# Kernel tuning notes

Measured on AMD Instinct MI355X. Metric: run time of the kernel, lower is better.

The kernel has to match this reference:

```python
import jax, jax.numpy as jnp
import numpy as np

N_SAMPLES = 2 ** 15          # 32768
STEP = 256                   # transform_step_size
WIN = 2048                   # transform/synthesis window
N_FRAMES = N_SAMPLES // STEP # 128
N_COEFFS = WIN // 2 + 1      # 1025
DILATIONS = (1, 2, 4, 8, 16, 32, 64, 1)


def hann(n):
    return 0.5 - 0.5 * jnp.cos(2.0 * jnp.pi * jnp.arange(n, dtype=jnp.float32) / n)


def transform(audio):
    # audio: (B, 1, N) -> magnitude STFT (B, 1024, 128)
    x = audio[:, 0, :]
    x = jnp.pad(x, ((0, 0), (0, WIN - STEP)))  # pad so n_frames == N_SAMPLES // STEP
    idx = np.arange(N_FRAMES)[:, None] * STEP + np.arange(WIN)[None, :]
    frames = x[:, idx] * hann(WIN)
    spec = jnp.abs(jnp.fft.rfft(frames, norm='ortho'))   # (B, F, 1025)
    return spec[..., : N_COEFFS - 1].transpose(0, 2, 1)  # (B, 1024, F)


def conv1x1(x, w, b):
    # x: (B, I, T), w: (O, I, 1), b: (O,)
    return jnp.einsum('oi,bit->bot', w[:, :, 0], x) + b[None, :, None]


def anticausal_block(x, w, b, dilation):
    # kernel_size=2 anti-causal dilated conv: looks at t and t+dilation (pad future)
    x_fut = jnp.pad(x, ((0, 0), (0, 0), (0, dilation)))[:, :, dilation:]
    y = (jnp.einsum('oi,bit->bot', w[:, :, 0], x)
         + jnp.einsum('oi,bit->bot', w[:, :, 1], x_fut)
         + b[None, :, None])
    y = jax.nn.leaky_relu(y, 0.2)
    y = y + x
    # do_norm: per-example max-norm
    y = y / (jnp.max(jnp.abs(y), axis=(1, 2), keepdims=True) + 1e-8)
    return y


def upsample_with_holes(x, desired_size):
    # zero-stuffing upsample: out[..., ::step] = x
    b, c, t = x.shape
    step = desired_size // t
    out = jnp.zeros((b, c, desired_size), x.dtype)
    return out.at[:, :, ::step].set(x)


def freq_domain_resonance(coeffs):
    # coeffs: (1, C, 1025) in [0, 1); per-frame decay = repeated spectral multiply
    c = jnp.clip(coeffs, 0.0, 0.9999)
    exps = jnp.arange(1, N_FRAMES + 1, dtype=coeffs.dtype)
    mags = c[:, :, None, :] ** exps[None, None, :, None]     # (1, C, F, 1025)
    frames = jnp.fft.irfft(mags, n=WIN) * hann(WIN)
    hop = WIN // 2
    total = hop * (N_FRAMES - 1) + WIN
    idx = np.arange(N_FRAMES)[:, None] * hop + np.arange(WIN)[None, :]
    out = jnp.zeros(frames.shape[:2] + (total,), frames.dtype)
    out = out.at[:, :, idx].add(frames)                      # overlap-add
    return out[..., :N_SAMPLES]                              # (1, C, N)


def fft_convolve(a, b):
    # circular-free conv via zero-padding to 2N, keep first N (matches repo fft_convolve)
    n = a.shape[-1]
    spec = jnp.fft.rfft(a, n=2 * n) * jnp.fft.rfft(b, n=2 * n)
    return jnp.fft.irfft(spec, n=2 * n)[..., :n]


def reference(audio, proj_in_w, proj_in_b, blocks_w, blocks_b,
              proj_sparse_w, proj_sparse_b, proj_dense_w, proj_dense_b, resonances):
    spec = transform(audio)                         # (B, 1024, 128)
    h = conv1x1(spec, proj_in_w, proj_in_b)         # (B, 32, 128)
    acc = jnp.zeros_like(h)
    for i, d in enumerate(DILATIONS):               # fixed 8-block stack
        h = anticausal_block(h, blocks_w[i], blocks_b[i], d)
        acc = acc + h
    x = conv1x1(acc, proj_sparse_w, proj_sparse_b)  # (B, 256, 128)
    sparse = jax.nn.relu(x)
    x = conv1x1(sparse, proj_dense_w, proj_dense_b) # (B, 32, 128)
    x = upsample_with_holes(x, N_SAMPLES)           # (B, 32, 32768)
    res = freq_domain_resonance(resonances)         # (1, 32, 32768), broadcast over B
    y = fft_convolve(x, res)                        # (B, 32, 32768)
    y = jnp.sum(y, axis=1, keepdims=True)           # (B, 1, 32768)
    return y, sparse


def setup_inputs() -> dict:
    key = jax.random.key(0)
    ks = jax.random.split(key, 12)
    u = lambda k, shape: jax.random.uniform(k, shape, jnp.float32, -0.05, 0.05)
    return {
        'audio': jax.random.normal(ks[0], (32, 1, N_SAMPLES), jnp.float32),
        'proj_in_w': u(ks[1], (32, 1024, 1)),
        'proj_in_b': jnp.zeros((32,), jnp.float32),
        'blocks_w': u(ks[2], (8, 32, 32, 2)),
        'blocks_b': jnp.zeros((8, 32), jnp.float32),
        'proj_sparse_w': u(ks[3], (256, 32, 1)),
        'proj_sparse_b': jnp.zeros((256,), jnp.float32),
        'proj_dense_w': u(ks[4], (32, 256, 1)),
        'proj_dense_b': jnp.zeros((32,), jnp.float32),
        'resonances': jax.random.uniform(ks[5], (1, 32, N_COEFFS), jnp.float32, 0.0, 1.0),
    }
```

## Files before the change

kernel.cpp:

```cpp
#include <hip/hip_runtime.h>

#define PI_F 3.14159265358979323846f

typedef short bf16x8 __attribute__((ext_vector_type(8)));
typedef float f32x4 __attribute__((ext_vector_type(4)));

#define MFMA16(acc, a, b) \
  acc = __builtin_amdgcn_mfma_f32_16x16x32_bf16(a, b, acc, 0, 0, 0)

#define WS_SPEC   0u
#define WS_H0     4194304u
#define WS_ACC    4325376u
#define WS_V      4456448u
#define WS_WTIN   4587520u
#define WS_WST    4620288u
#define WS_WDT    4628480u
#define WS_FRAMES 4636672u
#define WS_RES    6733824u

__device__ __forceinline__ void fft2048_stages(float2* buf, int tid) {
  for (int stage = 0; stage < 11; ++stage) {
    int half = 1 << stage;
    float base = -PI_F / (float)half;
    for (int t = tid; t < 1024; t += 256) {
      int j  = t & (half - 1);
      int i0 = ((t >> stage) << (stage + 1)) + j;
      int i1 = i0 + half;
      float s, c;
      __sincosf(base * (float)j, &s, &c);
      float2 u = buf[i0];
      float2 w = buf[i1];
      float tr = c * w.x - s * w.y;
      float ti = c * w.y + s * w.x;
      buf[i0] = make_float2(u.x + tr, u.y + ti);
      buf[i1] = make_float2(u.x - tr, u.y - ti);
    }
    __syncthreads();
  }
}

__global__ __launch_bounds__(256) void k_fft(const float* __restrict__ audio,
                                             const float* __restrict__ resin,
                                             float* __restrict__ spec,
                                             float* __restrict__ frames) {
  __shared__ float2 buf[2048];
  int blk = blockIdx.x;
  if (blk < 2048) {
    int b  = blk >> 6;
    int f0 = (blk & 63) * 2;
    for (int j = threadIdx.x; j < 2048; j += 256) {
      float h = 0.5f - 0.5f * __cosf(0.0030679615757712823f * (float)j);
      int i1 = f0 * 256 + j;
      int i2 = i1 + 256;
      float a1 = (i1 < 32768) ? audio[b * 32768 + i1] : 0.f;
      float a2 = (i2 < 32768) ? audio[b * 32768 + i2] : 0.f;
      buf[__brev((unsigned)j) >> 21] = make_float2(a1 * h, a2 * h);
    }
    __syncthreads();
    fft2048_stages(buf, threadIdx.x);
    const float scale = 0.5f * 0.022097086912079608f;
    for (int k = threadIdx.x; k < 1024; k += 256) {
      float2 zk = buf[k];
      float2 zn = buf[(2048 - k) & 2047];
      float f1r = zk.x + zn.x, f1i = zk.y - zn.y;
      float f2r = zk.y + zn.y, f2i = zk.x - zn.x;
      spec[(b * 128 + f0) * 1024 + k]     = sqrtf(f1r * f1r + f1i * f1i) * scale;
      spec[(b * 128 + f0 + 1) * 1024 + k] = sqrtf(f2r * f2r + f2i * f2i) * scale;
    }
  } else {
    int r = blk - 2048;
    int c = r >> 4;
    int g = r & 15;
    float e1 = (float)(2 * g + 1);
    for (int k = threadIdx.x; k < 2048; k += 256) {
      int kk = (k <= 1024) ? k : 2048 - k;
      float cv = resin[c * 1025 + kk];
      cv = fminf(fmaxf(cv, 0.f), 0.9999f);
      float m1 = __powf(cv, e1);
      float m2 = m1 * cv;
      buf[__brev((unsigned)k) >> 21] = make_float2(m1, m2);
    }
    __syncthreads();
    fft2048_stages(buf, threadIdx.x);
    for (int j = threadIdx.x; j < 2048; j += 256) {
      float h  = 0.5f - 0.5f * __cosf(0.0030679615757712823f * (float)j);
      float sc = h * (1.f / 2048.f);
      float2 z = buf[j];
      frames[(c * 32 + 2 * g) * 2048 + j]     = z.x * sc;
      frames[(c * 32 + 2 * g + 1) * 2048 + j] = z.y * sc;
    }
  }
}

__global__ __launch_bounds__(256) void k_prep(const float* __restrict__ Win,
                                              const float* __restrict__ Ws,
                                              const float* __restrict__ Wd,
                                              const float* __restrict__ bwIn,
                                              float* __restrict__ WT,
                                              float* __restrict__ WsT,
                                              float* __restrict__ WdT,
                                              short* __restrict__ Whg,
                                              short* __restrict__ Wlg) {
  int i = blockIdx.x * 256 + threadIdx.x;
  if (i < 32768) { int o = i >> 10, k = i & 1023; WT[k * 32 + o] = Win[i]; }
  if (i < 8192)  { int o2 = i >> 5, m = i & 31;   WsT[m * 256 + o2] = Ws[i]; }
  if (i < 8192)  { int c = i >> 8, o2 = i & 255;  WdT[o2 * 32 + c] = Wd[i]; }
  if (i < 16384) {
    int w = i & 1, m = (i >> 1) & 31, o = (i >> 6) & 31, s = i >> 11;
    float val = bwIn[i];
    unsigned bits = __float_as_uint(val);
    float rem = val - __uint_as_float(bits & 0xffff0000u);
    int row = (s * 2 + w) * 32 + o;
    Whg[row * 32 + m] = (short)(bits >> 16);
    Wlg[row * 32 + m] = (short)(__float_as_uint(rem) >> 16);
  }
}

__global__ __launch_bounds__(256) void k_proj_in(const float* __restrict__ spec,
                                                 const float* __restrict__ WT,
                                                 const float* __restrict__ bias,
                                                 float* __restrict__ h0) {
  __shared__ float specL[8][1024];
  __shared__ float red[32][8][8];
  int b  = blockIdx.x >> 4;
  int t0 = (blockIdx.x & 15) * 8;
  for (int i = threadIdx.x; i < 8192; i += 256) {
    int tt = i >> 10, k = i & 1023;
    specL[tt][k] = spec[(b * 128 + t0 + tt) * 1024 + k];
  }
  __syncthreads();
  int o = threadIdx.x & 31, p = threadIdx.x >> 5;
  float part[8] = {0.f,0.f,0.f,0.f,0.f,0.f,0.f,0.f};
  for (int i = 0; i < 128; ++i) {
    int k = p * 128 + ((i + p * 4) & 127);
    float w = WT[k * 32 + o];
#pragma unroll
    for (int tt = 0; tt < 8; ++tt) part[tt] += w * specL[tt][k];
  }
#pragma unroll
  for (int tt = 0; tt < 8; ++tt) red[o][tt][p] = part[tt];
  __syncthreads();
  int oo = threadIdx.x >> 3, tt2 = threadIdx.x & 7;
  float s = bias[oo];
#pragma unroll
  for (int p2 = 0; p2 < 8; ++p2) s += red[oo][tt2][p2];
  h0[b * 4096 + oo * 128 + t0 + tt2] = s;
}

__global__ __launch_bounds__(1024) void k_chain(const float* __restrict__ h0,
                                                const short* __restrict__ Whg,
                                                const short* __restrict__ Wlg,
                                                const float* __restrict__ bb,
                                                float* __restrict__ accout) {
  __shared__ __align__(16) short Hh[192 * 40];
  __shared__ __align__(16) short Hl[192 * 40];
  __shared__ float Hf[128 * 33];
  __shared__ float bL[256];
  __shared__ float red[16];
  int b = blockIdx.x, tid = threadIdx.x;

  for (int i = tid; i < 4096; i += 1024) {
    int t = i & 127;
    int o = i >> 7;
    float val = h0[b * 4096 + i];
    Hf[t * 33 + o] = val;
    unsigned bits = __float_as_uint(val);
    float rem = val - __uint_as_float(bits & 0xffff0000u);
    Hh[t * 40 + o] = (short)(bits >> 16);
    Hl[t * 40 + o] = (short)(__float_as_uint(rem) >> 16);
  }
  for (int i = tid; i < 64 * 40; i += 1024) {
    Hh[128 * 40 + i] = 0;
    Hl[128 * 40 + i] = 0;
  }
  if (tid < 256) bL[tid] = bb[tid];
  __syncthreads();

  int wave = tid >> 6, lane = tid & 63;
  int quad = lane >> 4, l15 = lane & 15;
  int t0 = (wave & 7) * 16, o0 = (wave >> 3) * 16;
  int tD = t0 + quad * 4;
  int oD = o0 + l15;

  const bf16x8* Hh8 = (const bf16x8*)Hh;
  const bf16x8* Hl8 = (const bf16x8*)Hl;
  const bf16x8* Wh8 = (const bf16x8*)Whg;
  const bf16x8* Wl8 = (const bf16x8*)Wlg;

  float accsum[4] = {0.f, 0.f, 0.f, 0.f};
  const int DIL[8] = {1, 2, 4, 8, 16, 32, 64, 1};

#pragma unroll
  for (int s = 0; s < 8; ++s) {
    int arow = t0 + l15;
    int frow = arow + DIL[s];
    bf16x8 Ah = Hh8[arow * 5 + quad];
    bf16x8 Al = Hl8[arow * 5 + quad];
    bf16x8 Fh = Hh8[frow * 5 + quad];
    bf16x8 Fl = Hl8[frow * 5 + quad];
    int w0row = ((s * 2 + 0) * 32 + oD) * 4 + quad;
    int w1row = ((s * 2 + 1) * 32 + oD) * 4 + quad;
    bf16x8 B0h = Wh8[w0row], B0l = Wl8[w0row];
    bf16x8 B1h = Wh8[w1row], B1l = Wl8[w1row];
    float bias = bL[s * 32 + oD];
    f32x4 acc = {bias, bias, bias, bias};
    MFMA16(acc, Ah, B0h); MFMA16(acc, Ah, B0l); MFMA16(acc, Al, B0h);
    MFMA16(acc, Fh, B1h); MFMA16(acc, Fh, B1l); MFMA16(acc, Fl, B1h);
    float hnew[4], lmax = 0.f;
#pragma unroll
    for (int r = 0; r < 4; ++r) {
      float sv = acc[r];
      sv = (sv > 0.f) ? sv : 0.2f * sv;
      sv += Hf[(tD + r) * 33 + oD];
      hnew[r] = sv;
      lmax = fmaxf(lmax, fabsf(sv));
    }
#pragma unroll
    for (int off = 32; off > 0; off >>= 1)
      lmax = fmaxf(lmax, __shfl_down(lmax, off, 64));
    if (lane == 0) red[wave] = lmax;
    __syncthreads();
    float mx = red[0];
#pragma unroll
    for (int i = 1; i < 16; ++i) mx = fmaxf(mx, red[i]);
    float nm = 1.f / (mx + 1e-8f);
#pragma unroll
    for (int r = 0; r < 4; ++r) {
      float hv = hnew[r] * nm;
      accsum[r] += hv;
      int t = tD + r;
      Hf[t * 33 + oD] = hv;
      unsigned bits = __float_as_uint(hv);
      float rem = hv - __uint_as_float(bits & 0xffff0000u);
      Hh[t * 40 + oD] = (short)(bits >> 16);
      Hl[t * 40 + oD] = (short)(__float_as_uint(rem) >> 16);
    }
    __syncthreads();
  }
#pragma unroll
  for (int r = 0; r < 4; ++r)
    accout[b * 4096 + (tD + r) * 32 + oD] = accsum[r];
}

__global__ __launch_bounds__(256) void k_sparse_dense(const float* __restrict__ acc,
                                                      const float* __restrict__ WsT,
                                                      const float* __restrict__ bs,
                                                      const float* __restrict__ WdT,
                                                      const float* __restrict__ bd,
                                                      float* __restrict__ out_sparse,
                                                      float* __restrict__ v) {
  __shared__ float accL[32];
  __shared__ float sL[256];
  __shared__ float red[8][32];
  int b = blockIdx.x >> 7, t = blockIdx.x & 127;
  int tid = threadIdx.x;
  if (tid < 32) accL[tid] = acc[b * 4096 + t * 32 + tid];
  __syncthreads();
  float s = bs[tid];
  for (int m = 0; m < 32; ++m) s += WsT[m * 256 + tid] * accL[m];
  s = fmaxf(s, 0.f);
  out_sparse[b * 32768 + tid * 128 + t] = s;
  sL[tid] = s;
  __syncthreads();
  int c = tid & 31, p = tid >> 5;
  float part = 0.f;
  for (int j = 0; j < 32; ++j) {
    int o2 = p * 32 + j;
    part += WdT[o2 * 32 + c] * sL[o2];
  }
  red[p][c] = part;
  __syncthreads();
  if (tid < 32) {
    float vv = bd[tid];
    for (int p2 = 0; p2 < 8; ++p2) vv += red[p2][tid];
    v[b * 4096 + tid * 128 + t] = vv;
  }
}

__global__ __launch_bounds__(256) void k_res_assemble(const float* __restrict__ frames,
                                                      float* __restrict__ res) {
  int i = blockIdx.x * 256 + threadIdx.x;
  int c = i >> 15, s = i & 32767;
  int g = s >> 10, j0 = s & 1023;
  float v = frames[(c * 32 + g) * 2048 + j0];
  if (g > 0) v += frames[(c * 32 + g - 1) * 2048 + j0 + 1024];
  res[i] = v;
}

__global__ __launch_bounds__(256) void k_bpack(const float* __restrict__ res,
                                               short* __restrict__ Bh,
                                               short* __restrict__ Bl) {
  int c = blockIdx.x >> 4, o = blockIdx.x & 15;
  int r = threadIdx.x;
  bf16x8 hv, lv;
#pragma unroll
  for (int j = 0; j < 8; ++j) {
    float val = res[c * 32768 + (8 * o + j) * 256 + r];
    unsigned bits = __float_as_uint(val);
    float rem = val - __uint_as_float(bits & 0xffff0000u);
    hv[j] = (short)(bits >> 16);
    lv[j] = (short)(__float_as_uint(rem) >> 16);
  }
  int unit = (blockIdx.x * 16 + (r >> 4)) * 16 + (r & 15);
  ((bf16x8*)Bh)[unit] = hv;
  ((bf16x8*)Bl)[unit] = lv;
}

__global__ __launch_bounds__(512, 4) void k_conv(const float* __restrict__ v,
                                                 const short* __restrict__ Bh,
                                                 const short* __restrict__ Bl,
                                                 float* __restrict__ y) {
  __shared__ __align__(16) short AH[32 * 264];
  __shared__ __align__(16) short AL[32 * 264];
  __shared__ float vwin[2][16][48];

  int blk = blockIdx.x;
  int b = blk / 20;
  int e = blk - b * 20;
  int j, uc;
  if      (e < 2)  { j = 0; uc = e; }
  else if (e < 6)  { j = 1; uc = e - 2; }
  else if (e < 12) { j = 2; uc = e - 6; }
  else             { j = 3; uc = e - 12; }
  int D0 = 32 * j - 16 * uc;

  for (int i = threadIdx.x; i < 1504; i += 512) {
    int ii = i % 47;
    int r  = i / 47;
    int c  = r & 15, p = r >> 4;
    int d  = D0 - 15 + ii;
    vwin[p][c][ii] = (d >= 0 && d < 128)
        ? v[b * 4096 + (16 * p + c) * 128 + d] : 0.f;
  }
  __syncthreads();

  int lane = threadIdx.x & 63, wave = threadIdx.x >> 6;
  int quad = lane >> 4, l15 = lane & 15;
  int cq   = quad >> 1;
  int og   = 2 * uc + (quad & 1);
  int nt0  = wave * 2;

  f32x4 acc00 = (f32x4)0.f, acc01 = (f32x4)0.f;
  f32x4 acc10 = (f32x4)0.f, acc11 = (f32x4)0.f;

  const bf16x8* AH8 = (const bf16x8*)AH;
  const bf16x8* AL8 = (const bf16x8*)AL;
  const bf16x8* Bh8 = (const bf16x8*)Bh;
  const bf16x8* Bl8 = (const bf16x8*)Bl;
  short2* AH2 = (short2*)AH;
  short2* AL2 = (short2*)AL;

  int abase0 = (0 * 16 + l15) * 33 + quad;
  int abase1 = (1 * 16 + l15) * 33 + quad;

  for (int p = 0; p < 2; ++p) {
    for (int i = threadIdx.x; i < 4096; i += 512) {
      int kk2 = i & 127;
      int row = i >> 7;
      int cl  = kk2 >> 3;
      int uu  = (kk2 & 7) * 2;
      int ii  = row - uu + 15;
      float v0 = vwin[p][cl][ii];
      float v1 = vwin[p][cl][ii - 1];
      unsigned w0 = __float_as_uint(v0), w1 = __float_as_uint(v1);
      float r0 = v0 - __uint_as_float(w0 & 0xffff0000u);
      float r1 = v1 - __uint_as_float(w1 & 0xffff0000u);
      int u2 = row * 132 + kk2;
      AH2[u2] = make_short2((short)(w0 >> 16), (short)(w1 >> 16));
      AL2[u2] = make_short2((short)(__float_as_uint(r0) >> 16),
                            (short)(__float_as_uint(r1) >> 16));
    }
    __syncthreads();

#pragma unroll
    for (int ks = 0; ks < 8; ++ks) {
      bf16x8 ah0 = AH8[abase0 + ks * 4];
      bf16x8 al0 = AL8[abase0 + ks * 4];
      bf16x8 ah1 = AH8[abase1 + ks * 4];
      bf16x8 al1 = AL8[abase1 + ks * 4];
      int c   = 16 * p + 2 * ks + cq;
      int bb0 = (c * 16 + og) * 256 + l15;
      bf16x8 bh0 = Bh8[bb0 + nt0 * 16];
      bf16x8 bl0 = Bl8[bb0 + nt0 * 16];
      bf16x8 bh1 = Bh8[bb0 + (nt0 + 1) * 16];
      bf16x8 bl1 = Bl8[bb0 + (nt0 + 1) * 16];
      MFMA16(acc00, ah0, bh0); MFMA16(acc00, ah0, bl0); MFMA16(acc00, al0, bh0);
      MFMA16(acc10, ah1, bh0); MFMA16(acc10, ah1, bl0); MFMA16(acc10, al1, bh0);
      MFMA16(acc01, ah0, bh1); MFMA16(acc01, ah0, bl1); MFMA16(acc01, al0, bh1);
      MFMA16(acc11, ah1, bh1); MFMA16(acc11, ah1, bl1); MFMA16(acc11, al1, bh1);
    }
    __syncthreads();
  }

  {
    float* yb0 = y + b * 32768 + (32 * j + 0 * 16 + quad * 4) * 256 + l15;
    float* yb1 = y + b * 32768 + (32 * j + 1 * 16 + quad * 4) * 256 + l15;
#pragma unroll
    for (int reg = 0; reg < 4; ++reg) {
      atomicAdd(yb0 + reg * 256 + (nt0 + 0) * 16, acc00[reg]);
      atomicAdd(yb0 + reg * 256 + (nt0 + 1) * 16, acc01[reg]);
      atomicAdd(yb1 + reg * 256 + (nt0 + 0) * 16, acc10[reg]);
      atomicAdd(yb1 + reg * 256 + (nt0 + 1) * 16, acc11[reg]);
    }
  }
}

extern "C" void kernel_launch(void* const* d_in, const int* in_sizes, int n_in,
                              void* d_out, int out_size, void* d_ws, size_t ws_size,
                              hipStream_t stream) {
  const float* audio = (const float*)d_in[0];
  const float* Win   = (const float*)d_in[1];
  const float* bin   = (const float*)d_in[2];
  const float* bw    = (const float*)d_in[3];
  const float* bb    = (const float*)d_in[4];
  const float* Ws    = (const float*)d_in[5];
  const float* bs    = (const float*)d_in[6];
  const float* Wd    = (const float*)d_in[7];
  const float* bd    = (const float*)d_in[8];
  const float* reson = (const float*)d_in[9];

  float* out = (float*)d_out;
  float* ws  = (float*)d_ws;

  float* spec   = ws + WS_SPEC;
  float* h0     = ws + WS_H0;
  float* accb   = ws + WS_ACC;
  float* vbuf   = ws + WS_V;
  float* WT     = ws + WS_WTIN;
  float* WsT    = ws + WS_WST;
  float* WdT    = ws + WS_WDT;
  float* frames = ws + WS_FRAMES;
  float* resbuf = ws + WS_RES;
  short* Bh = (short*)(ws + WS_FRAMES);
  short* Bl = (short*)(ws + WS_FRAMES + 524288u);
  short* Whg = (short*)(ws + WS_V);
  short* Wlg = (short*)(ws + WS_V + 8192u);

  hipMemsetAsync(d_out, 0, 1048576u * sizeof(float), stream);

  k_prep<<<128, 256, 0, stream>>>(Win, Ws, Wd, bw, WT, WsT, WdT, Whg, Wlg);
  k_fft<<<2560, 256, 0, stream>>>(audio, reson, spec, frames);
  k_res_assemble<<<4096, 256, 0, stream>>>(frames, resbuf);
  k_bpack<<<512, 256, 0, stream>>>(resbuf, Bh, Bl);
  k_proj_in<<<512, 256, 0, stream>>>(spec, WT, bin, h0);
  k_chain<<<32, 1024, 0, stream>>>(h0, Whg, Wlg, bb, accb);
  k_sparse_dense<<<4096, 256, 0, stream>>>(accb, WsT, bs, WdT, bd, out + 1048576, vbuf);
  k_conv<<<640, 512, 0, stream>>>(vbuf, Bh, Bl, out);
}
```

Measured before the change: 202.7 us.

## Fuse resonance overlap-add into bf16 packing, batch sparse/dense over four frames, remap conv blocks

The separate overlap-add kernel is folded into the bf16 hi/lo packing kernel, so the intermediate resonance buffer is no longer written and then read back, and one launch is removed. The sparse/dense projection kernel now handles four time steps per block, reusing each weight load across them and launching a quarter as many blocks. The k_conv block index is remapped so that blocks sharing the same resonance slice are grouped by XCD, aiming at better L2 reuse of the packed B operand. Bh/Bl move to the WS_RES region because frames must stay intact while packing reads it.

```diff
diff --git a/kernel.cpp b/kernel.cpp
--- a/kernel.cpp
+++ b/kernel.cpp
@@ -249,53 +249,59 @@
                                                       const float* __restrict__ bd,
                                                       float* __restrict__ out_sparse,
                                                       float* __restrict__ v) {
-  __shared__ float accL[32];
-  __shared__ float sL[256];
-  __shared__ float red[8][32];
-  int b = blockIdx.x >> 7, t = blockIdx.x & 127;
+  __shared__ float accL[4][32];
+  __shared__ float sL[4][256];
+  __shared__ float red[8][4][32];
+  int b = blockIdx.x >> 5, tq = blockIdx.x & 31;
+  int t0 = tq * 4;
   int tid = threadIdx.x;
-  if (tid < 32) accL[tid] = acc[b * 4096 + t * 32 + tid];
-  __syncthreads();
-  float s = bs[tid];
-  for (int m = 0; m < 32; ++m) s += WsT[m * 256 + tid] * accL[m];
-  s = fmaxf(s, 0.f);
-  out_sparse[b * 32768 + tid * 128 + t] = s;
-  sL[tid] = s;
+  if (tid < 128)
+    accL[tid >> 5][tid & 31] = acc[b * 4096 + (t0 + (tid >> 5)) * 32 + (tid & 31)];
+  __syncthreads();
+  float bsv = bs[tid];
+  float s0 = bsv, s1 = bsv, s2 = bsv, s3 = bsv;
+  for (int m = 0; m < 32; ++m) {
+    float w = WsT[m * 256 + tid];
+    s0 += w * accL[0][m]; s1 += w * accL[1][m];
+    s2 += w * accL[2][m]; s3 += w * accL[3][m];
+  }
+  s0 = fmaxf(s0, 0.f); s1 = fmaxf(s1, 0.f); s2 = fmaxf(s2, 0.f); s3 = fmaxf(s3, 0.f);
+  float* os = out_sparse + b * 32768 + tid * 128 + t0;
+  os[0] = s0; os[1] = s1; os[2] = s2; os[3] = s3;
+  sL[0][tid] = s0; sL[1][tid] = s1; sL[2][tid] = s2; sL[3][tid] = s3;
   __syncthreads();
   int c = tid & 31, p = tid >> 5;
-  float part = 0.f;
-  for (int j = 0; j < 32; ++j) {
-    int o2 = p * 32 + j;
-    part += WdT[o2 * 32 + c] * sL[o2];
-  }
-  red[p][c] = part;
-  __syncthreads();
-  if (tid < 32) {
-    float vv = bd[tid];
-    for (int p2 = 0; p2 < 8; ++p2) vv += red[p2][tid];
-    v[b * 4096 + tid * 128 + t] = vv;
-  }
-}
-
-__global__ __launch_bounds__(256) void k_res_assemble(const float* __restrict__ frames,
-                                                      float* __restrict__ res) {
-  int i = blockIdx.x * 256 + threadIdx.x;
-  int c = i >> 15, s = i & 32767;
-  int g = s >> 10, j0 = s & 1023;
-  float v = frames[(c * 32 + g) * 2048 + j0];
-  if (g > 0) v += frames[(c * 32 + g - 1) * 2048 + j0 + 1024];
-  res[i] = v;
-}
-
-__global__ __launch_bounds__(256) void k_bpack(const float* __restrict__ res,
-                                               short* __restrict__ Bh,
-                                               short* __restrict__ Bl) {
+  float p0 = 0.f, p1 = 0.f, p2 = 0.f, p3 = 0.f;
+  for (int jj = 0; jj < 32; ++jj) {
+    int o2 = p * 32 + jj;
+    float w = WdT[o2 * 32 + c];
+    p0 += w * sL[0][o2]; p1 += w * sL[1][o2];
+    p2 += w * sL[2][o2]; p3 += w * sL[3][o2];
+  }
+  red[p][0][c] = p0; red[p][1][c] = p1; red[p][2][c] = p2; red[p][3][c] = p3;
+  __syncthreads();
+  if (tid < 128) {
+    int tt = tid >> 5, cc = tid & 31;
+    float vv = bd[cc];
+#pragma unroll
+    for (int p2i = 0; p2i < 8; ++p2i) vv += red[p2i][tt][cc];
+    v[b * 4096 + cc * 128 + t0 + tt] = vv;
+  }
+}
+
+__global__ __launch_bounds__(256) void k_obpack(const float* __restrict__ frames,
+                                                short* __restrict__ Bh,
+                                                short* __restrict__ Bl) {
   int c = blockIdx.x >> 4, o = blockIdx.x & 15;
   int r = threadIdx.x;
   bf16x8 hv, lv;
 #pragma unroll
   for (int j = 0; j < 8; ++j) {
-    float val = res[c * 32768 + (8 * o + j) * 256 + r];
+    int fo = 8 * o + j;
+    int g  = fo >> 2;
+    int j0 = ((fo & 3) << 8) + r;
+    float val = frames[(c * 32 + g) * 2048 + j0];
+    if (g > 0) val += frames[(c * 32 + g - 1) * 2048 + j0 + 1024];
     unsigned bits = __float_as_uint(val);
     float rem = val - __uint_as_float(bits & 0xffff0000u);
     hv[j] = (short)(bits >> 16);
@@ -314,9 +320,13 @@
   __shared__ __align__(16) short AL[32 * 264];
   __shared__ float vwin[2][16][48];
 
-  int blk = blockIdx.x;
-  int b = blk / 20;
-  int e = blk - b * 20;
+  int xcd  = blockIdx.x & 7;
+  int slot = blockIdx.x >> 3;
+  int e, b;
+  if      (slot < 32) { e = xcd;      b = slot; }
+  else if (slot < 64) { e = xcd + 8;  b = slot - 32; }
+  else                { e = (xcd < 4) ? (xcd + 16) : (xcd + 12);
+                        b = (xcd < 4) ? (slot - 64) : (slot - 48); }
   int j, uc;
   if      (e < 2)  { j = 0; uc = e; }
   else if (e < 6)  { j = 1; uc = e - 2; }
@@ -327,10 +337,10 @@
   for (int i = threadIdx.x; i < 1504; i += 512) {
     int ii = i % 47;
     int r  = i / 47;
-    int c  = r & 15, p = r >> 4;
+    int c  = r & 15, ph = r >> 4;
     int d  = D0 - 15 + ii;
-    vwin[p][c][ii] = (d >= 0 && d < 128)
-        ? v[b * 4096 + (16 * p + c) * 128 + d] : 0.f;
+    vwin[ph][c][ii] = (d >= 0 && d < 128)
+        ? v[b * 4096 + (16 * ph + c) * 128 + d] : 0.f;
   }
   __syncthreads();
 
@@ -430,9 +440,8 @@
   float* WsT    = ws + WS_WST;
   float* WdT    = ws + WS_WDT;
   float* frames = ws + WS_FRAMES;
-  float* resbuf = ws + WS_RES;
-  short* Bh = (short*)(ws + WS_FRAMES);
-  short* Bl = (short*)(ws + WS_FRAMES + 524288u);
+  short* Bh = (short*)(ws + WS_RES);
+  short* Bl = (short*)(ws + WS_RES + 524288u);
   short* Whg = (short*)(ws + WS_V);
   short* Wlg = (short*)(ws + WS_V + 8192u);
 
@@ -440,10 +449,9 @@
 
   k_prep<<<128, 256, 0, stream>>>(Win, Ws, Wd, bw, WT, WsT, WdT, Whg, Wlg);
   k_fft<<<2560, 256, 0, stream>>>(audio, reson, spec, frames);
-  k_res_assemble<<<4096, 256, 0, stream>>>(frames, resbuf);
-  k_bpack<<<512, 256, 0, stream>>>(resbuf, Bh, Bl);
+  k_obpack<<<512, 256, 0, stream>>>(frames, Bh, Bl);
   k_proj_in<<<512, 256, 0, stream>>>(spec, WT, bin, h0);
   k_chain<<<32, 1024, 0, stream>>>(h0, Whg, Wlg, bb, accb);
-  k_sparse_dense<<<4096, 256, 0, stream>>>(accb, WsT, bs, WdT, bd, out + 1048576, vbuf);
+  k_sparse_dense<<<1024, 256, 0, stream>>>(accb, WsT, bs, WdT, bd, out + 1048576, vbuf);
   k_conv<<<640, 512, 0, stream>>>(vbuf, Bh, Bl, out);
 }
```

New measurement: 189.5 us. 6.5% less time.
